# Kernel tuning notes

Hardware: AMD Instinct MI355X
Metric: run time of the kernel (lower is better)

## Reference

```python
import jax, jax.numpy as jnp
import numpy as np
from itertools import product as _prod

B = 2          # batch size
NPB = 4096     # voxels per batch
C = 384        # input_dim
H = 8          # num_heads
OUT = 32       # output_dim (seg classes)
SPATIAL = (32, 256, 256)
POOL_R = np.array([1, 2, 2, 2])    # [1]+query_gs_ratio
COMP_R = np.array([1, 16, 16, 16])  # [1]+compress_ratio


def _coords():
    rng = np.random.default_rng(0)
    rows = []
    for b in range(B):
        cand = np.stack([rng.integers(0, s, 4 * NPB) for s in SPATIAL], 1)
        cand = np.unique(cand, axis=0)
        sel = cand[rng.permutation(len(cand))[:NPB]]
        rows.append(np.concatenate([np.full((NPB, 1), b, np.int64), sel], 1))
    return np.concatenate(rows).astype(np.int32)


def setup_inputs() -> dict:
    idx = _coords()                     # [N,4] unique (b,z,y,x)
    N = idx.shape[0]
    pool_u, pool_inv = np.unique(idx // POOL_R, axis=0, return_inverse=True)
    emb_u, emb_inv = np.unique(idx // COMP_R, axis=0, return_inverse=True)
    # submanifold 3x3x3 neighbor table (same batch), -1 = missing
    lut = {tuple(r): i for i, r in enumerate(idx.tolist())}
    nbr = np.full((N, 27), -1, np.int32)
    rows = idx.tolist()
    for k, (dz, dy, dx) in enumerate(_prod((-1, 0, 1), repeat=3)):
        for i, (b, z, y, x) in enumerate(rows):
            nbr[i, k] = lut.get((b, z + dz, y + dy, x + dx), -1)
    key = jax.random.key(0)
    ks = jax.random.split(key, 12)
    g = lambda k, shp, s: jax.random.normal(k, shp, jnp.float32) * s
    s = 1.0 / float(np.sqrt(C))
    return dict(
        feats=g(ks[0], (N, C), 1.0),
        W_pool=g(ks[1], (C, C), s), b_pool=jnp.zeros((C,), jnp.float32),
        W_emb=g(ks[2], (C, C), s), b_emb=jnp.zeros((C,), jnp.float32),
        Wq=g(ks[3], (C, C), s), bq=jnp.zeros((C,), jnp.float32),
        Wk=g(ks[4], (C, C), s), bk=jnp.zeros((C,), jnp.float32),
        Wv=g(ks[5], (C, C), s), bv=jnp.zeros((C,), jnp.float32),
        Wo=g(ks[6], (C, C), s), bo=jnp.zeros((C,), jnp.float32),
        W_conv=g(ks[7], (27, C, OUT), 1.0 / float(np.sqrt(27 * C))),
        b_conv=jnp.zeros((OUT,), jnp.float32),
        pool_inv=jnp.asarray(pool_inv, jnp.int32),
        pool_coords=jnp.asarray(pool_u, jnp.int32),
        emb_inv=jnp.asarray(emb_inv, jnp.int32),
        emb_coords=jnp.asarray(emb_u, jnp.int32),
        nbr_idx=jnp.asarray(nbr),
        batch_size=B,
    )


def _sine_pe(xyz, d_pos):
    # xyz: [n,3] normalized to [0,1]; PositionEmbeddingCoordsSine (3detr-style)
    cdim = d_pos // xyz.shape[1]
    dim_t = 10000.0 ** (2.0 * (jnp.arange(cdim) // 2).astype(jnp.float32) / cdim)
    emb = (xyz * (2.0 * jnp.pi))[:, :, None] / dim_t          # [n,3,cdim]
    pe = jnp.stack([jnp.sin(emb[..., 0::2]), jnp.cos(emb[..., 1::2])], -1)
    return pe.reshape(xyz.shape[0], -1)                        # [n,d_pos]


def reference(feats, W_pool, b_pool, W_emb, b_emb, Wq, bq, Wk, bk, Wv, bv,
              Wo, bo, W_conv, b_conv, pool_inv, pool_coords, emb_inv,
              emb_coords, nbr_idx, batch_size):
    Mp, Me, Cc = pool_coords.shape[0], emb_coords.shape[0], feats.shape[1]
    hd = Cc // H
    # query path: linear + scatter_max over pool cells
    pool_f = jax.ops.segment_max(feats @ W_pool + b_pool, pool_inv, num_segments=Mp)
    # kv path: linear + scatter_max over compressed cells (coords of argmax rows
    # within a cell all equal the unique cell coord, so mean == unique coord)
    emb_f = jax.ops.segment_max(feats @ W_emb + b_emb, emb_inv, num_segments=Me)
    # per-batch min/max-normalized sine positional encoding on concat(emb,pool)
    emb_xyz = emb_coords[:, 1:].astype(jnp.float32)
    pool_xyz = pool_coords[:, 1:].astype(jnp.float32)
    all_xyz = jnp.concatenate([emb_xyz, pool_xyz], 0)
    bids = jnp.concatenate([emb_coords[:, 0], pool_coords[:, 0]], 0)
    mins = jax.ops.segment_min(all_xyz, bids, num_segments=batch_size)
    maxs = jax.ops.segment_max(all_xyz, bids, num_segments=batch_size)
    norm = (all_xyz - mins[bids]) / (maxs[bids] - mins[bids] + 1e-6)
    pe = _sine_pe(norm, Cc)
    emb_f = emb_f + pe[:Me]
    pool_f = pool_f + pe[Me:]
    # multi-head cross-attention, masked to same-batch pairs
    q = (pool_f @ Wq + bq).reshape(Mp, H, hd)
    k = (emb_f @ Wk + bk).reshape(Me, H, hd)
    v = (emb_f @ Wv + bv).reshape(Me, H, hd)
    scores = jnp.einsum('phd,ehd->hpe', q, k) / jnp.sqrt(jnp.float32(hd))
    same_b = pool_coords[:, 0][None, :, None] == emb_coords[:, 0][None, None, :]
    attn = jax.nn.softmax(jnp.where(same_b, scores, -1e9), axis=-1)
    o = jnp.einsum('hpe,ehd->phd', attn, v).reshape(Mp, Cc) @ Wo + bo
    # broadcast back to voxels + residual
    new_f = feats + o[pool_inv]
    # SubMConv3d seg head: gather 27 neighbors, contract with kernel
    valid = (nbr_idx >= 0)[:, :, None]
    gathered = jnp.where(valid, new_f[jnp.maximum(nbr_idx, 0)], 0.0)  # [N,27,C]
    logits = jnp.einsum('nkc,kco->no', gathered, W_conv) + b_conv
    return logits
```

## Files before the change

kernel.cpp:

```cpp
#include <hip/hip_runtime.h>
#include <hip/hip_bf16.h>
#include <math.h>

#define CDIM 384
#define NHEAD 8
#define HD 48
#define OUTD 32
#define MAXB 16
#define CONVK 10368

typedef __bf16 bf16x8 __attribute__((ext_vector_type(8)));
typedef float f32x4 __attribute__((ext_vector_type(4)));

__device__ __forceinline__ f32x4 mfma16(bf16x8 a, bf16x8 b, f32x4 c) {
  return __builtin_amdgcn_mfma_f32_16x16x32_bf16(a, b, c, 0, 0, 0);
}
__device__ __forceinline__ bf16x8 zero8() {
  bf16x8 z = {(__bf16)0.f, (__bf16)0.f, (__bf16)0.f, (__bf16)0.f,
              (__bf16)0.f, (__bf16)0.f, (__bf16)0.f, (__bf16)0.f};
  return z;
}

__device__ __forceinline__ unsigned enc_f(float f) {
  unsigned u = __float_as_uint(f);
  return (u & 0x80000000u) ? ~u : (u | 0x80000000u);
}
__device__ __forceinline__ float dec_f(unsigned u) {
  unsigned v = (u & 0x80000000u) ? (u ^ 0x80000000u) : ~u;
  return __uint_as_float(v);
}

__global__ void init_small_kernel(int* smin, int* smax, int* eb) {
  int t = threadIdx.x;
  if (t < MAXB * 3) { smin[t] = 0x7fffffff; smax[t] = (int)0x80000000; }
  if (t <= MAXB) eb[t] = 0;
}

__global__ __launch_bounds__(256) void prep_kernel(
    const float* __restrict__ feats, __hip_bfloat16* __restrict__ feats16, int N,
    const float* __restrict__ W_pool, const float* __restrict__ W_emb,
    const float* __restrict__ Wk, const float* __restrict__ Wv,
    const float* __restrict__ Wq, const float* __restrict__ Wo,
    __hip_bfloat16* __restrict__ Wt_pe, __hip_bfloat16* __restrict__ Wt_kv,
    __hip_bfloat16* __restrict__ Wt_q, __hip_bfloat16* __restrict__ Wt_o,
    const float* __restrict__ Wc, __hip_bfloat16* __restrict__ Wct,
    unsigned* __restrict__ encA, unsigned* __restrict__ encB,
    __hip_bfloat16* __restrict__ vt, int Mepad,
    const int* __restrict__ ec, const int* __restrict__ pc, int Mp, int Me,
    const int* __restrict__ bsz, int* smin, int* smax, int* ebv,
    int nbF, int nbW, int nbC, int nbZA, int nbZB, int nbVt, int nbM) {
  __shared__ int lmin[MAXB * 3], lmax[MAXB * 3];
  int b = blockIdx.x;
  int t = threadIdx.x;
  if (b < nbF) {
    int v = b * 256 + t;
    if (v < N * 48) {
      float4 a0 = *reinterpret_cast<const float4*>(feats + (size_t)v * 8);
      float4 a1 = *reinterpret_cast<const float4*>(feats + (size_t)v * 8 + 4);
      __hip_bfloat16 tmp[8] = {
        __float2bfloat16(a0.x), __float2bfloat16(a0.y), __float2bfloat16(a0.z), __float2bfloat16(a0.w),
        __float2bfloat16(a1.x), __float2bfloat16(a1.y), __float2bfloat16(a1.z), __float2bfloat16(a1.w)};
      *reinterpret_cast<bf16x8*>(feats16 + (size_t)v * 8) = *reinterpret_cast<const bf16x8*>(tmp);
    }
    return;
  }
  b -= nbF;
  if (b < 6 * nbW) {
    int m = b / nbW;
    int v = (b - m * nbW) * 256 + t;
    if (v >= CDIM * 48) return;
    const float* src;
    __hip_bfloat16* dst;
    switch (m) {
      case 0: src = W_pool; dst = Wt_pe; break;
      case 1: src = W_emb;  dst = Wt_pe + (size_t)CDIM * CDIM; break;
      case 2: src = Wk;     dst = Wt_kv; break;
      case 3: src = Wv;     dst = Wt_kv + (size_t)CDIM * CDIM; break;
      case 4: src = Wq;     dst = Wt_q; break;
      default: src = Wo;    dst = Wt_o; break;
    }
    int k8i = v / CDIM;
    int n = v - k8i * CDIM;
    int k8 = k8i * 8;
    __hip_bfloat16 tmp[8];
    #pragma unroll
    for (int u = 0; u < 8; ++u) tmp[u] = __float2bfloat16(src[(size_t)(k8 + u) * CDIM + n]);
    *reinterpret_cast<bf16x8*>(dst + (size_t)n * CDIM + k8) = *reinterpret_cast<const bf16x8*>(tmp);
    return;
  }
  b -= 6 * nbW;
  if (b < nbC) {
    int v = b * 256 + t;
    if (v >= OUTD * (CONVK / 8)) return;
    int k8i = v >> 5;
    int n = v & 31;
    int k8 = k8i * 8;
    __hip_bfloat16 tmp[8];
    #pragma unroll
    for (int u = 0; u < 8; ++u) tmp[u] = __float2bfloat16(Wc[(size_t)(k8 + u) * OUTD + n]);
    *reinterpret_cast<bf16x8*>(Wct + (size_t)n * CONVK + k8) = *reinterpret_cast<const bf16x8*>(tmp);
    return;
  }
  b -= nbC;
  if (b < nbZA) {
    size_t v = (size_t)b * 256 + t;
    if (v < (size_t)Mp * 96) {
      uint4 z = {0u, 0u, 0u, 0u};
      reinterpret_cast<uint4*>(encA)[v] = z;
    }
    return;
  }
  b -= nbZA;
  if (b < nbZB) {
    size_t v = (size_t)b * 256 + t;
    if (v < (size_t)Me * 96) {
      uint4 z = {0u, 0u, 0u, 0u};
      reinterpret_cast<uint4*>(encB)[v] = z;
    }
    return;
  }
  b -= nbZB;
  if (b < nbVt) {
    int v = b * 256 + t;
    int g = Mepad >> 3;
    if (v < 512 * g) {
      int row = v / g;
      int c8 = (v - row * g) * 8;
      __hip_bfloat16 bv = __float2bfloat16(((row & 63) == HD) ? 1.0f : 0.0f);
      __hip_bfloat16 tmp[8] = {bv, bv, bv, bv, bv, bv, bv, bv};
      *reinterpret_cast<bf16x8*>(vt + (size_t)row * Mepad + c8) =
          *reinterpret_cast<const bf16x8*>(tmp);
    }
    return;
  }
  b -= nbVt;
  if (b < nbM) {
    if (t < MAXB * 3) { lmin[t] = 0x7fffffff; lmax[t] = (int)0x80000000; }
    __syncthreads();
    int i = b * 256 + t;
    int tot = Me + Mp;
    if (i < tot) {
      const int* r = (i < Me) ? (ec + 4 * i) : (pc + 4 * (i - Me));
      int bb = r[0];
      #pragma unroll
      for (int d = 0; d < 3; ++d) {
        atomicMin(&lmin[bb * 3 + d], r[1 + d]);
        atomicMax(&lmax[bb * 3 + d], r[1 + d]);
      }
    }
    __syncthreads();
    if (t < MAXB * 3) {
      if (lmin[t] != 0x7fffffff) atomicMin(&smin[t], lmin[t]);
      if (lmax[t] != (int)0x80000000) atomicMax(&smax[t], lmax[t]);
    }
    return;
  }
  b -= nbM;
  {
    int e = b * 256 + t;
    if (e == 0) { ebv[0] = 0; ebv[bsz[0]] = Me; }
    if (e > 0 && e < Me) {
      int b0 = ec[4 * (e - 1)], b1 = ec[4 * e];
      for (int bb = b0 + 1; bb <= b1; ++bb) ebv[bb] = e;
    }
  }
}

__global__ void pe_kernel(const unsigned* __restrict__ encP, const unsigned* __restrict__ encE,
                          __hip_bfloat16* __restrict__ pool16, __hip_bfloat16* __restrict__ emb16,
                          const int* __restrict__ pc, int Mp,
                          const int* __restrict__ ec, int Me,
                          const int* __restrict__ smin, const int* __restrict__ smax) {
  int gid = blockIdx.x * blockDim.x + threadIdx.x;
  int total = (Mp + Me) * CDIM;
  if (gid >= total) return;
  int row = gid / CDIM, c = gid - row * CDIM;
  const int* coords;
  const unsigned* src;
  __hip_bfloat16* dst;
  int lrow;
  if (row < Me) { lrow = row; coords = ec + 4 * row; src = encE; dst = emb16; }
  else { lrow = row - Me; coords = pc + 4 * lrow; src = encP; dst = pool16; }
  int b = coords[0];
  int dim = c >> 7;
  int i = c & 127;
  int j = i >> 1;
  float x = (float)coords[1 + dim];
  float mn = (float)smin[b * 3 + dim];
  float mx = (float)smax[b * 3 + dim];
  float nrm = (x - mn) / (mx - mn + 1e-6f);
  float freq = exp2f(-(float)j * 0.20762050593046014f);
  float arg = nrm * 6.283185307179586f * freq;
  float pe = (i & 1) ? __cosf(arg) : __sinf(arg);
  float val = dec_f(src[(size_t)lrow * CDIM + c]) + pe;
  dst[(size_t)lrow * CDIM + c] = __float2bfloat16(val);
}

template <int EPI>
__device__ __forceinline__ void mgemm_body(
    int bx, int by,
    __hip_bfloat16 (*As)[72], __hip_bfloat16 (*Bs)[72],
    const __hip_bfloat16* __restrict__ A, int M,
    const __hip_bfloat16* __restrict__ Wt,
    const float* __restrict__ bias0, const float* __restrict__ bias1,
    void* __restrict__ d0, void* __restrict__ d1,
    const int* __restrict__ inv0, const int* __restrict__ inv1,
    int Mepad) {
  const int m0 = bx * 128;
  const int n0 = by * 64;
  const int t = threadIdx.x;
  const int lane = t & 63, w = t >> 6;
  const int wr = w >> 1, wc = w & 1;
  const int lq = lane & 15, lg = lane >> 4;

  f32x4 acc[4][2];
  #pragma unroll
  for (int i = 0; i < 4; ++i) {
    acc[i][0] = (f32x4){0.f, 0.f, 0.f, 0.f};
    acc[i][1] = (f32x4){0.f, 0.f, 0.f, 0.f};
  }
  const int arow = t >> 3;
  const int acol = (t & 7) * 8;

  for (int k0 = 0; k0 < CDIM; k0 += 64) {
    #pragma unroll
    for (int i = 0; i < 4; ++i) {
      int r = arow + i * 32;
      int gr = m0 + r;
      bf16x8 val = zero8();
      if (gr < M) val = *reinterpret_cast<const bf16x8*>(A + (size_t)gr * CDIM + k0 + acol);
      *reinterpret_cast<bf16x8*>(&As[r][acol]) = val;
    }
    #pragma unroll
    for (int i = 0; i < 2; ++i) {
      int r = arow + i * 32;
      bf16x8 val = *reinterpret_cast<const bf16x8*>(Wt + (size_t)(n0 + r) * CDIM + k0 + acol);
      *reinterpret_cast<bf16x8*>(&Bs[r][acol]) = val;
    }
    __syncthreads();
    #pragma unroll
    for (int ks = 0; ks < 2; ++ks) {
      bf16x8 af[4], bfv[2];
      #pragma unroll
      for (int fm = 0; fm < 4; ++fm)
        af[fm] = *reinterpret_cast<const bf16x8*>(&As[wr * 64 + fm * 16 + lq][ks * 32 + lg * 8]);
      #pragma unroll
      for (int fn = 0; fn < 2; ++fn)
        bfv[fn] = *reinterpret_cast<const bf16x8*>(&Bs[wc * 32 + fn * 16 + lq][ks * 32 + lg * 8]);
      #pragma unroll
      for (int fm = 0; fm < 4; ++fm)
        #pragma unroll
        for (int fn = 0; fn < 2; ++fn)
          acc[fm][fn] = mfma16(af[fm], bfv[fn], acc[fm][fn]);
    }
    __syncthreads();
  }

  const bool sec = (n0 >= CDIM);
  const int nb = n0 - (sec ? CDIM : 0) + wc * 32;
  const int nA = nb + lq, nB = nb + 16 + lq;

  if (EPI == 0) {
    const float* bias = sec ? bias1 : bias0;
    unsigned* dst = (unsigned*)(sec ? d1 : d0);
    const int* inv = sec ? inv1 : inv0;
    float bA = bias[nA], bB = bias[nB];
    #pragma unroll
    for (int fm = 0; fm < 4; ++fm) {
      int rbase = m0 + wr * 64 + fm * 16 + lg * 4;
      int cs = -1;
      float mA = 0.f, mB = 0.f;
      #pragma unroll
      for (int j = 0; j < 4; ++j) {
        int r = rbase + j;
        if (r < M) {
          int s = inv[r];
          float vA = acc[fm][0][j] + bA;
          float vB = acc[fm][1][j] + bB;
          if (s == cs) { mA = fmaxf(mA, vA); mB = fmaxf(mB, vB); }
          else {
            if (cs >= 0) {
              atomicMax(&dst[(size_t)cs * CDIM + nA], enc_f(mA));
              atomicMax(&dst[(size_t)cs * CDIM + nB], enc_f(mB));
            }
            cs = s; mA = vA; mB = vB;
          }
        }
      }
      if (cs >= 0) {
        atomicMax(&dst[(size_t)cs * CDIM + nA], enc_f(mA));
        atomicMax(&dst[(size_t)cs * CDIM + nB], enc_f(mB));
      }
    }
  } else if (EPI == 1) {
    float bA = bias0[nA], bB = bias0[nB];
    float* dst = (float*)d0;
    #pragma unroll
    for (int fm = 0; fm < 4; ++fm)
      #pragma unroll
      for (int j = 0; j < 4; ++j) {
        int r = m0 + wr * 64 + fm * 16 + lg * 4 + j;
        if (r < M) {
          dst[(size_t)r * CDIM + nA] = acc[fm][0][j] + bA;
          dst[(size_t)r * CDIM + nB] = acc[fm][1][j] + bB;
        }
      }
  } else if (EPI == 2) {
    const float scale = 0.2082350914f;
    float bA = bias0[nA], bB = bias0[nB];
    int hA = nA / HD, dA = nA - hA * HD;
    int hB = nB / HD, dB = nB - hB * HD;
    __hip_bfloat16* dst = (__hip_bfloat16*)d0;
    #pragma unroll
    for (int fm = 0; fm < 4; ++fm)
      #pragma unroll
      for (int j = 0; j < 4; ++j) {
        int r = m0 + wr * 64 + fm * 16 + lg * 4 + j;
        if (r < M) {
          dst[(size_t)r * 512 + hA * 64 + dA] = __float2bfloat16((acc[fm][0][j] + bA) * scale);
          dst[(size_t)r * 512 + hB * 64 + dB] = __float2bfloat16((acc[fm][1][j] + bB) * scale);
        }
      }
  } else {
    if (!sec) {
      float bA = bias0[nA], bB = bias0[nB];
      int hA = nA / HD, dA = nA - hA * HD;
      int hB = nB / HD, dB = nB - hB * HD;
      __hip_bfloat16* dst = (__hip_bfloat16*)d0;
      #pragma unroll
      for (int fm = 0; fm < 4; ++fm)
        #pragma unroll
        for (int j = 0; j < 4; ++j) {
          int r = m0 + wr * 64 + fm * 16 + lg * 4 + j;
          if (r < M) {
            dst[(size_t)r * 512 + hA * 64 + dA] = __float2bfloat16(acc[fm][0][j] + bA);
            dst[(size_t)r * 512 + hB * 64 + dB] = __float2bfloat16(acc[fm][1][j] + bB);
          }
        }
    } else {
      float bA = bias1[nA], bB = bias1[nB];
      int hA = nA / HD, dA = nA - hA * HD;
      int hB = nB / HD, dB = nB - hB * HD;
      __hip_bfloat16* dst = (__hip_bfloat16*)d1;
      #pragma unroll
      for (int fm = 0; fm < 4; ++fm)
        #pragma unroll
        for (int j = 0; j < 4; ++j) {
          int r = m0 + wr * 64 + fm * 16 + lg * 4 + j;
          if (r < M) {
            dst[(size_t)(hA * 64 + dA) * Mepad + r] = __float2bfloat16(acc[fm][0][j] + bA);
            dst[(size_t)(hB * 64 + dB) * Mepad + r] = __float2bfloat16(acc[fm][1][j] + bB);
          }
        }
    }
  }
  if ((EPI == 2 || EPI == 3) && n0 == 0) {
    __hip_bfloat16* dst = (__hip_bfloat16*)d0;
    for (int c = t; c < 1024; c += 256) {
      int r = m0 + (c >> 3);
      int hh = c & 7;
      if (r < M) {
        bf16x8 z = zero8();
        *reinterpret_cast<bf16x8*>(dst + (size_t)r * 512 + hh * 64 + 48) = z;
        *reinterpret_cast<bf16x8*>(dst + (size_t)r * 512 + hh * 64 + 56) = z;
      }
    }
  }
}

__global__ __launch_bounds__(256) void mgemm0_kernel(
    const __hip_bfloat16* __restrict__ A, int M, const __hip_bfloat16* __restrict__ Wt,
    const float* __restrict__ bias0, const float* __restrict__ bias1,
    unsigned* __restrict__ d0, unsigned* __restrict__ d1,
    const int* __restrict__ inv0, const int* __restrict__ inv1) {
  __shared__ __align__(16) __hip_bfloat16 As[128][72];
  __shared__ __align__(16) __hip_bfloat16 Bs[64][72];
  mgemm_body<0>(blockIdx.x, blockIdx.y, As, Bs, A, M, Wt, bias0, bias1, d0, d1, inv0, inv1, 0);
}

__global__ __launch_bounds__(256) void mgemm1_kernel(
    const __hip_bfloat16* __restrict__ A, int M, const __hip_bfloat16* __restrict__ Wt,
    const float* __restrict__ bias0, float* __restrict__ d0) {
  __shared__ __align__(16) __hip_bfloat16 As[128][72];
  __shared__ __align__(16) __hip_bfloat16 Bs[64][72];
  mgemm_body<1>(blockIdx.x, blockIdx.y, As, Bs, A, M, Wt, bias0, nullptr, d0, nullptr, nullptr, nullptr, 0);
}

__global__ __launch_bounds__(256) void qkv_kernel(
    const __hip_bfloat16* __restrict__ pool16, int Mp, const __hip_bfloat16* __restrict__ Wt_q,
    const float* __restrict__ bq,
    const __hip_bfloat16* __restrict__ emb16, int Me, const __hip_bfloat16* __restrict__ Wt_kv,
    const float* __restrict__ bk, const float* __restrict__ bv,
    __hip_bfloat16* __restrict__ q16, __hip_bfloat16* __restrict__ k16,
    __hip_bfloat16* __restrict__ vt, int Mepad, int nbQ, int gxQ, int gxK) {
  __shared__ __align__(16) __hip_bfloat16 As[128][72];
  __shared__ __align__(16) __hip_bfloat16 Bs[64][72];
  int b = blockIdx.x;
  if (b < nbQ) {
    mgemm_body<2>(b % gxQ, b / gxQ, As, Bs, pool16, Mp, Wt_q, bq, nullptr,
                  q16, nullptr, nullptr, nullptr, 0);
  } else {
    b -= nbQ;
    mgemm_body<3>(b % gxK, b / gxK, As, Bs, emb16, Me, Wt_kv, bk, bv,
                  k16, vt, nullptr, nullptr, Mepad);
  }
}

__global__ __launch_bounds__(256) void attn_mfma_kernel(
    const __hip_bfloat16* __restrict__ qb, const __hip_bfloat16* __restrict__ kb,
    const __hip_bfloat16* __restrict__ vt, int Mepad,
    const int* __restrict__ pc, const int* __restrict__ eb,
    int Mp, int Me, __hip_bfloat16* __restrict__ ob) {
  __shared__ __align__(16) __hip_bfloat16 Ks[2][64][72];
  __shared__ __align__(16) __hip_bfloat16 Vs[2][64][72];
  __shared__ __align__(16) __hip_bfloat16 pl[4][16][72];
  __shared__ int sred[4][4];
  const int h = blockIdx.y;
  const int t = threadIdx.x;
  const int wv = t >> 6, lane = t & 63;
  const int lq = lane & 15, lg = lane >> 4;
  const int q0 = blockIdx.x * 64 + wv * 16;

  int lo[4], hi[4];
  #pragma unroll
  for (int r = 0; r < 4; ++r) {
    int q = q0 + lg * 4 + r;
    if (q < Mp) { int b = pc[4 * q]; lo[r] = eb[b]; hi[r] = eb[b + 1]; }
    else { lo[r] = 0x7fffffff; hi[r] = 0; }
  }
  int lomin = min(min(lo[0], lo[1]), min(lo[2], lo[3]));
  int lomax = max(max(lo[0], lo[1]), max(lo[2], lo[3]));
  int himin = min(min(hi[0], hi[1]), min(hi[2], hi[3]));
  int himax = max(max(hi[0], hi[1]), max(hi[2], hi[3]));
  #pragma unroll
  for (int off = 1; off < 64; off <<= 1) {
    lomin = min(lomin, __shfl_xor(lomin, off));
    lomax = max(lomax, __shfl_xor(lomax, off));
    himin = min(himin, __shfl_xor(himin, off));
    himax = max(himax, __shfl_xor(himax, off));
  }
  if (lane == 0) {
    sred[wv][0] = lomin; sred[wv][1] = lomax;
    sred[wv][2] = himin; sred[wv][3] = himax;
  }
  __syncthreads();
  lomin = min(min(sred[0][0], sred[1][0]), min(sred[2][0], sred[3][0]));
  lomax = max(max(sred[0][1], sred[1][1]), max(sred[2][1], sred[3][1]));
  himin = min(min(sred[0][2], sred[1][2]), min(sred[2][2], sred[3][2]));
  himax = max(max(sred[0][3], sred[1][3]), max(sred[2][3], sred[3][3]));

  int qrow = min(q0 + lq, Mp - 1);
  const __hip_bfloat16* qp = qb + (size_t)qrow * 512 + h * 64 + lg * 8;
  bf16x8 aq0 = *reinterpret_cast<const bf16x8*>(qp);
  bf16x8 aq1 = *reinterpret_cast<const bf16x8*>(qp + 32);

  const int str = t >> 2;
  const int stc = (t & 3) * 16;
  const __hip_bfloat16* vrow = vt + (size_t)(h * 64 + str) * Mepad + stc;

  f32x4 zero = {0.f, 0.f, 0.f, 0.f};
  f32x4 oacc[4];
  oacc[0] = zero; oacc[1] = zero; oacc[2] = zero; oacc[3] = zero;

  bf16x8 k0, k1, v0, v1;
  auto load_tile = [&](int e0) {
    int er = e0 + str;
    k0 = zero8(); k1 = zero8();
    if (er < Me) {
      const __hip_bfloat16* kp = kb + (size_t)er * 512 + h * 64 + stc;
      k0 = *reinterpret_cast<const bf16x8*>(kp);
      k1 = *reinterpret_cast<const bf16x8*>(kp + 8);
    }
    v0 = *reinterpret_cast<const bf16x8*>(vrow + e0);
    v1 = *reinterpret_cast<const bf16x8*>(vrow + e0 + 8);
  };
  auto store_tile = [&](int nb) {
    *reinterpret_cast<bf16x8*>(&Ks[nb][str][stc]) = k0;
    *reinterpret_cast<bf16x8*>(&Ks[nb][str][stc + 8]) = k1;
    *reinterpret_cast<bf16x8*>(&Vs[nb][str][stc]) = v0;
    *reinterpret_cast<bf16x8*>(&Vs[nb][str][stc + 8]) = v1;
  };
  const int e0beg = lomin & ~63;
  load_tile(e0beg);
  store_tile(0);
  if (e0beg + 64 < himax) load_tile(e0beg + 64);

  int it = 0;
  for (int e0 = e0beg; e0 < himax; e0 += 64, ++it) {
    __syncthreads();
    const int cur = it & 1;
    if (e0 + 64 < himax) {
      store_tile(cur ^ 1);
      if (e0 + 128 < himax) load_tile(e0 + 128);
    }

    f32x4 sf[4];
    #pragma unroll
    for (int s = 0; s < 4; ++s) {
      bf16x8 bk0 = *reinterpret_cast<const bf16x8*>(&Ks[cur][s * 16 + lq][lg * 8]);
      bf16x8 bk1 = *reinterpret_cast<const bf16x8*>(&Ks[cur][s * 16 + lq][32 + lg * 8]);
      f32x4 z = zero;
      z = mfma16(aq0, bk0, z);
      z = mfma16(aq1, bk1, z);
      sf[s] = z;
    }
    const bool interior = (e0 >= lomax) && (e0 + 64 <= himin);
    if (interior) {
      #pragma unroll
      for (int s = 0; s < 4; ++s)
        #pragma unroll
        for (int r = 0; r < 4; ++r)
          pl[wv][lg * 4 + r][s * 16 + lq] = __float2bfloat16(exp2f(sf[s][r]));
    } else {
      #pragma unroll
      for (int s = 0; s < 4; ++s) {
        int e = e0 + s * 16 + lq;
        #pragma unroll
        for (int r = 0; r < 4; ++r) {
          bool m = (e >= lo[r]) && (e < hi[r]);
          float p = m ? exp2f(sf[s][r]) : 0.f;
          pl[wv][lg * 4 + r][s * 16 + lq] = __float2bfloat16(p);
        }
      }
    }
    asm volatile("s_waitcnt lgkmcnt(0)" ::: "memory");
    __builtin_amdgcn_sched_barrier(0);
    #pragma unroll
    for (int ks = 0; ks < 2; ++ks) {
      bf16x8 ap = *reinterpret_cast<const bf16x8*>(&pl[wv][lq][ks * 32 + lg * 8]);
      #pragma unroll
      for (int dt = 0; dt < 4; ++dt) {
        bf16x8 bv = *reinterpret_cast<const bf16x8*>(&Vs[cur][dt * 16 + lq][ks * 32 + lg * 8]);
        oacc[dt] = mfma16(ap, bv, oacc[dt]);
      }
    }
  }

  #pragma unroll
  for (int r = 0; r < 4; ++r) {
    float l = __shfl(oacc[3][r], (lane & 48));
    int q = q0 + lg * 4 + r;
    if (q < Mp && l > 0.f) {
      float inv = 1.0f / l;
      __hip_bfloat16* op = ob + (size_t)q * CDIM + h * HD;
      op[lq]      = __float2bfloat16(oacc[0][r] * inv);
      op[16 + lq] = __float2bfloat16(oacc[1][r] * inv);
      op[32 + lq] = __float2bfloat16(oacc[2][r] * inv);
    }
  }
}

__global__ void newf16_kernel(const float* __restrict__ feats, const float* __restrict__ o2,
                              const int* __restrict__ pinv, __hip_bfloat16* __restrict__ nf,
                              int N) {
  int v = blockIdx.x * 256 + threadIdx.x;
  if (v >= N * 48) return;
  int n = v / 48, c8 = (v - n * 48) * 8;
  const float* fp = feats + (size_t)n * CDIM + c8;
  const float* op = o2 + (size_t)pinv[n] * CDIM + c8;
  float4 a0 = *reinterpret_cast<const float4*>(fp);
  float4 a1 = *reinterpret_cast<const float4*>(fp + 4);
  float4 b0 = *reinterpret_cast<const float4*>(op);
  float4 b1 = *reinterpret_cast<const float4*>(op + 4);
  __hip_bfloat16 tmp[8] = {
    __float2bfloat16(a0.x + b0.x), __float2bfloat16(a0.y + b0.y),
    __float2bfloat16(a0.z + b0.z), __float2bfloat16(a0.w + b0.w),
    __float2bfloat16(a1.x + b1.x), __float2bfloat16(a1.y + b1.y),
    __float2bfloat16(a1.z + b1.z), __float2bfloat16(a1.w + b1.w)};
  *reinterpret_cast<bf16x8*>(nf + (size_t)v * 8) = *reinterpret_cast<const bf16x8*>(tmp);
}

__global__ __launch_bounds__(256) void mconv_kernel(
    const __hip_bfloat16* __restrict__ nf, const int* __restrict__ nbr,
    const __hip_bfloat16* __restrict__ Wct, float* __restrict__ outp, int N) {
  __shared__ __align__(16) __hip_bfloat16 As[128][72];
  __shared__ __align__(16) __hip_bfloat16 Bs[32][72];
  __shared__ int jrow[128];
  const int n0 = blockIdx.x * 128;
  const int kg = blockIdx.y;
  const int t = threadIdx.x;
  const int lane = t & 63, w = t >> 6;
  const int lq = lane & 15, lg = lane >> 4;
  f32x4 acc[2][2];
  acc[0][0] = (f32x4){0.f,0.f,0.f,0.f}; acc[0][1] = acc[0][0];
  acc[1][0] = acc[0][0]; acc[1][1] = acc[0][0];
  const int arow = t >> 3, acol = (t & 7) * 8;

  for (int kk = kg * 3; kk < kg * 3 + 3; ++kk) {
    __syncthreads();
    if (t < 128) {
      int n = n0 + t;
      jrow[t] = (n < N) ? nbr[(size_t)n * 27 + kk] : -1;
    }
    __syncthreads();
    for (int c0 = 0; c0 < CDIM; c0 += 64) {
      #pragma unroll
      for (int i = 0; i < 4; ++i) {
        int r = arow + i * 32;
        int j = jrow[r];
        bf16x8 val = zero8();
        if (j >= 0) val = *reinterpret_cast<const bf16x8*>(nf + (size_t)j * CDIM + c0 + acol);
        *reinterpret_cast<bf16x8*>(&As[r][acol]) = val;
      }
      {
        int r = t >> 3;
        bf16x8 val = *reinterpret_cast<const bf16x8*>(Wct + (size_t)r * CONVK + kk * CDIM + c0 + acol);
        *reinterpret_cast<bf16x8*>(&Bs[r][acol]) = val;
      }
      __syncthreads();
      #pragma unroll
      for (int ks = 0; ks < 2; ++ks) {
        bf16x8 af[2], bfv[2];
        #pragma unroll
        for (int fm = 0; fm < 2; ++fm)
          af[fm] = *reinterpret_cast<const bf16x8*>(&As[w * 32 + fm * 16 + lq][ks * 32 + lg * 8]);
        #pragma unroll
        for (int fn = 0; fn < 2; ++fn)
          bfv[fn] = *reinterpret_cast<const bf16x8*>(&Bs[fn * 16 + lq][ks * 32 + lg * 8]);
        #pragma unroll
        for (int fm = 0; fm < 2; ++fm)
          #pragma unroll
          for (int fn = 0; fn < 2; ++fn)
            acc[fm][fn] = mfma16(af[fm], bfv[fn], acc[fm][fn]);
      }
      __syncthreads();
    }
  }
  #pragma unroll
  for (int fm = 0; fm < 2; ++fm)
    #pragma unroll
    for (int j = 0; j < 4; ++j) {
      int r = n0 + w * 32 + fm * 16 + lg * 4 + j;
      if (r < N) {
        #pragma unroll
        for (int fn = 0; fn < 2; ++fn)
          outp[((size_t)kg * N + r) * OUTD + fn * 16 + lq] = acc[fm][fn][j];
      }
    }
}

__global__ void conv_reduce_kernel(const float* __restrict__ outp,
                                   const float* __restrict__ bc,
                                   float* __restrict__ out, int N) {
  int v = blockIdx.x * 256 + threadIdx.x;
  if (v >= N * OUTD) return;
  int oo = v & (OUTD - 1);
  float s = bc[oo];
  #pragma unroll
  for (int kg = 0; kg < 9; ++kg) s += outp[(size_t)kg * N * OUTD + v];
  out[v] = s;
}

extern "C" void kernel_launch(void* const* d_in, const int* in_sizes, int n_in,
                              void* d_out, int out_size, void* d_ws, size_t ws_size,
                              hipStream_t stream) {
  const float* feats  = (const float*)d_in[0];
  const float* W_pool = (const float*)d_in[1];
  const float* b_pool = (const float*)d_in[2];
  const float* W_emb  = (const float*)d_in[3];
  const float* b_emb  = (const float*)d_in[4];
  const float* Wq = (const float*)d_in[5];  const float* bq = (const float*)d_in[6];
  const float* Wk = (const float*)d_in[7];  const float* bk = (const float*)d_in[8];
  const float* Wv = (const float*)d_in[9];  const float* bv = (const float*)d_in[10];
  const float* Wo = (const float*)d_in[11]; const float* bo = (const float*)d_in[12];
  const float* Wc = (const float*)d_in[13]; const float* bc = (const float*)d_in[14];
  const int* pool_inv    = (const int*)d_in[15];
  const int* pool_coords = (const int*)d_in[16];
  const int* emb_inv     = (const int*)d_in[17];
  const int* emb_coords  = (const int*)d_in[18];
  const int* nbr         = (const int*)d_in[19];
  const int* bsz         = (const int*)d_in[20];
  int N  = in_sizes[0] / CDIM;
  int Mp = in_sizes[16] / 4;
  int Me = in_sizes[18] / 4;
  int Mepad = ((Me >> 6) + 2) << 6;

  char* wsb = (char*)d_ws;
  size_t off = 0;
  auto alloc = [&](size_t bytes) { void* p = wsb + off; off += (bytes + 255) & ~(size_t)255; return p; };
  unsigned* encA = (unsigned*)alloc((size_t)Mp * CDIM * 4);
  unsigned* encB = (unsigned*)alloc((size_t)Me * CDIM * 4);
  __hip_bfloat16* vt = (__hip_bfloat16*)alloc((size_t)512 * Mepad * 2);
  __hip_bfloat16* pool16  = (__hip_bfloat16*)alloc((size_t)Mp * CDIM * 2);
  __hip_bfloat16* emb16   = (__hip_bfloat16*)alloc((size_t)Me * CDIM * 2);
  __hip_bfloat16* feats16 = (__hip_bfloat16*)alloc((size_t)N * CDIM * 2);
  float* o2 = (float*)alloc((size_t)Mp * CDIM * 4 > (size_t)9 * N * OUTD * 4
                                ? (size_t)Mp * CDIM * 4 : (size_t)9 * N * OUTD * 4);
  __hip_bfloat16* Wt_pe = (__hip_bfloat16*)alloc((size_t)768 * CDIM * 2);
  __hip_bfloat16* Wt_kv = (__hip_bfloat16*)alloc((size_t)768 * CDIM * 2);
  __hip_bfloat16* Wt_q  = (__hip_bfloat16*)alloc((size_t)CDIM * CDIM * 2);
  __hip_bfloat16* Wt_o  = (__hip_bfloat16*)alloc((size_t)CDIM * CDIM * 2);
  __hip_bfloat16* Wct   = (__hip_bfloat16*)alloc((size_t)OUTD * CONVK * 2);
  int* smin = (int*)alloc(MAXB * 3 * 4);
  int* smax = (int*)alloc(MAXB * 3 * 4);
  int* eb   = (int*)alloc((MAXB + 1) * 4);

  __hip_bfloat16* q16  = (__hip_bfloat16*)encA;
  __hip_bfloat16* k16  = (__hip_bfloat16*)encB;
  __hip_bfloat16* ob16 = pool16;
  __hip_bfloat16* newf16 = feats16;
  float* outp = o2;

  init_small_kernel<<<1, 64, 0, stream>>>(smin, smax, eb);

  int nbF  = (N * 48 + 255) / 256;
  int nbW  = (CDIM * 48 + 255) / 256;
  int nbC  = (OUTD * (CONVK / 8) + 255) / 256;
  int nbZA = ((Mp * 96) + 255) / 256;
  int nbZB = ((Me * 96) + 255) / 256;
  int nbVt = ((512 * (Mepad >> 3)) + 255) / 256;
  int nbM  = (Mp + Me + 255) / 256;
  int nbE  = (Me + 255) / 256;
  prep_kernel<<<nbF + 6 * nbW + nbC + nbZA + nbZB + nbVt + nbM + nbE, 256, 0, stream>>>(
      feats, feats16, N, W_pool, W_emb, Wk, Wv, Wq, Wo,
      Wt_pe, Wt_kv, Wt_q, Wt_o, Wc, Wct, encA, encB, vt, Mepad,
      emb_coords, pool_coords, Mp, Me, bsz, smin, smax, eb,
      nbF, nbW, nbC, nbZA, nbZB, nbVt, nbM);

  mgemm0_kernel<<<dim3((N + 127) / 128, 12), 256, 0, stream>>>(
      feats16, N, Wt_pe, b_pool, b_emb, encA, encB, pool_inv, emb_inv);
  pe_kernel<<<((Mp + Me) * CDIM + 255) / 256, 256, 0, stream>>>(
      encA, encB, pool16, emb16, pool_coords, Mp, emb_coords, Me, smin, smax);

  {
    int gxQ = (Mp + 127) / 128, gxK = (Me + 127) / 128;
    int nbQ = gxQ * 6;
    qkv_kernel<<<nbQ + gxK * 12, 256, 0, stream>>>(
        pool16, Mp, Wt_q, bq, emb16, Me, Wt_kv, bk, bv,
        q16, k16, vt, Mepad, nbQ, gxQ, gxK);
  }

  attn_mfma_kernel<<<dim3((Mp + 63) / 64, NHEAD), 256, 0, stream>>>(
      q16, k16, vt, Mepad, pool_coords, eb, Mp, Me, ob16);

  mgemm1_kernel<<<dim3((Mp + 127) / 128, 6), 256, 0, stream>>>(
      ob16, Mp, Wt_o, bo, o2);

  newf16_kernel<<<(N * 48 + 255) / 256, 256, 0, stream>>>(feats, o2, pool_inv, newf16, N);

  mconv_kernel<<<dim3((N + 127) / 128, 9), 256, 0, stream>>>(newf16, nbr, Wct, outp, N);
  conv_reduce_kernel<<<(N * OUTD + 255) / 256, 256, 0, stream>>>(outp, bc, (float*)d_out, N);
}
```

Measured before the change: 158.9 us.

## Split attention key range across two blocks and merge partials in a combine kernel

Adds a grid z-dimension of two so each attention block handles half of the key tiles for its query group. Each half writes unnormalised fp32 partial outputs, including the denominator column, to a new workspace buffer. A new combine kernel adds the two partials and divides by the summed denominator to produce the bf16 output. The aim is to shorten each block's serial key loop and add parallelism, at the cost of an extra kernel launch and extra fp32 partial-output traffic.

```diff
diff --git a/kernel.cpp b/kernel.cpp
--- a/kernel.cpp
+++ b/kernel.cpp
@@ -358,11 +358,11 @@
     __hip_bfloat16* dst = (__hip_bfloat16*)d0;
     for (int c = t; c < 1024; c += 256) {
       int r = m0 + (c >> 3);
-      int hh = c & 7;
+      int hx = c & 7;
       if (r < M) {
         bf16x8 z = zero8();
-        *reinterpret_cast<bf16x8*>(dst + (size_t)r * 512 + hh * 64 + 48) = z;
-        *reinterpret_cast<bf16x8*>(dst + (size_t)r * 512 + hh * 64 + 56) = z;
+        *reinterpret_cast<bf16x8*>(dst + (size_t)r * 512 + hx * 64 + 48) = z;
+        *reinterpret_cast<bf16x8*>(dst + (size_t)r * 512 + hx * 64 + 56) = z;
       }
     }
   }
@@ -410,12 +410,13 @@
     const __hip_bfloat16* __restrict__ qb, const __hip_bfloat16* __restrict__ kb,
     const __hip_bfloat16* __restrict__ vt, int Mepad,
     const int* __restrict__ pc, const int* __restrict__ eb,
-    int Mp, int Me, __hip_bfloat16* __restrict__ ob) {
+    int Mp, int Me, float* __restrict__ po) {
   __shared__ __align__(16) __hip_bfloat16 Ks[2][64][72];
   __shared__ __align__(16) __hip_bfloat16 Vs[2][64][72];
   __shared__ __align__(16) __hip_bfloat16 pl[4][16][72];
   __shared__ int sred[4][4];
   const int h = blockIdx.y;
+  const int zz = blockIdx.z;
   const int t = threadIdx.x;
   const int wv = t >> 6, lane = t & 63;
   const int lq = lane & 15, lg = lane >> 4;
@@ -449,6 +450,12 @@
   himin = min(min(sred[0][2], sred[1][2]), min(sred[2][2], sred[3][2]));
   himax = max(max(sred[0][3], sred[1][3]), max(sred[2][3], sred[3][3]));
 
+  const int e0all = lomin & ~63;
+  const int nt = (himax > e0all) ? ((himax - e0all + 63) >> 6) : 0;
+  const int half = (nt + 1) >> 1;
+  const int s0 = e0all + zz * half * 64;
+  const int send = min(himax, e0all + (zz ? nt : half) * 64);
+
   int qrow = min(q0 + lq, Mp - 1);
   const __hip_bfloat16* qp = qb + (size_t)qrow * 512 + h * 64 + lg * 8;
   bf16x8 aq0 = *reinterpret_cast<const bf16x8*>(qp);
@@ -480,18 +487,19 @@
     *reinterpret_cast<bf16x8*>(&Vs[nb][str][stc]) = v0;
     *reinterpret_cast<bf16x8*>(&Vs[nb][str][stc + 8]) = v1;
   };
-  const int e0beg = lomin & ~63;
-  load_tile(e0beg);
-  store_tile(0);
-  if (e0beg + 64 < himax) load_tile(e0beg + 64);
+  if (s0 < send) {
+    load_tile(s0);
+    store_tile(0);
+    if (s0 + 64 < send) load_tile(s0 + 64);
+  }
 
   int it = 0;
-  for (int e0 = e0beg; e0 < himax; e0 += 64, ++it) {
+  for (int e0 = s0; e0 < send; e0 += 64, ++it) {
     __syncthreads();
     const int cur = it & 1;
-    if (e0 + 64 < himax) {
+    if (e0 + 64 < send) {
       store_tile(cur ^ 1);
-      if (e0 + 128 < himax) load_tile(e0 + 128);
+      if (e0 + 128 < send) load_tile(e0 + 128);
     }
 
     f32x4 sf[4];
@@ -538,16 +546,26 @@
 
   #pragma unroll
   for (int r = 0; r < 4; ++r) {
-    float l = __shfl(oacc[3][r], (lane & 48));
     int q = q0 + lg * 4 + r;
-    if (q < Mp && l > 0.f) {
-      float inv = 1.0f / l;
-      __hip_bfloat16* op = ob + (size_t)q * CDIM + h * HD;
-      op[lq]      = __float2bfloat16(oacc[0][r] * inv);
-      op[16 + lq] = __float2bfloat16(oacc[1][r] * inv);
-      op[32 + lq] = __float2bfloat16(oacc[2][r] * inv);
-    }
-  }
+    if (q < Mp) {
+      float* pp = po + (((size_t)zz * Mp + q) * NHEAD + h) * 64;
+      #pragma unroll
+      for (int dt = 0; dt < 4; ++dt) pp[dt * 16 + lq] = oacc[dt][r];
+    }
+  }
+}
+
+__global__ void combine_kernel(const float* __restrict__ po, int Mp,
+                               __hip_bfloat16* __restrict__ ob) {
+  int gid = blockIdx.x * 256 + threadIdx.x;
+  if (gid >= Mp * CDIM) return;
+  int q = gid / CDIM, c = gid - q * CDIM;
+  int h = c / HD, d = c - h * HD;
+  const float* p0 = po + (((size_t)q) * NHEAD + h) * 64;
+  const float* p1 = po + (((size_t)(Mp + q)) * NHEAD + h) * 64;
+  float l = p0[HD] + p1[HD];
+  float v = p0[d] + p1[d];
+  ob[(size_t)q * CDIM + c] = __float2bfloat16(l > 0.f ? v / l : 0.f);
 }
 
 __global__ void newf16_kernel(const float* __restrict__ feats, const float* __restrict__ o2,
@@ -691,6 +709,7 @@
   __hip_bfloat16* Wt_q  = (__hip_bfloat16*)alloc((size_t)CDIM * CDIM * 2);
   __hip_bfloat16* Wt_o  = (__hip_bfloat16*)alloc((size_t)CDIM * CDIM * 2);
   __hip_bfloat16* Wct   = (__hip_bfloat16*)alloc((size_t)OUTD * CONVK * 2);
+  float* po = (float*)alloc((size_t)2 * Mp * NHEAD * 64 * 4);
   int* smin = (int*)alloc(MAXB * 3 * 4);
   int* smax = (int*)alloc(MAXB * 3 * 4);
   int* eb   = (int*)alloc((MAXB + 1) * 4);
@@ -730,8 +749,9 @@
         q16, k16, vt, Mepad, nbQ, gxQ, gxK);
   }
 
-  attn_mfma_kernel<<<dim3((Mp + 63) / 64, NHEAD), 256, 0, stream>>>(
-      q16, k16, vt, Mepad, pool_coords, eb, Mp, Me, ob16);
+  attn_mfma_kernel<<<dim3((Mp + 63) / 64, NHEAD, 2), 256, 0, stream>>>(
+      q16, k16, vt, Mepad, pool_coords, eb, Mp, Me, po);
+  combine_kernel<<<(Mp * CDIM + 255) / 256, 256, 0, stream>>>(po, Mp, ob16);
 
   mgemm1_kernel<<<dim3((Mp + 127) / 128, 6), 256, 0, stream>>>(
       ob16, Mp, Wt_o, bo, o2);
```

New measurement: 168.4 us. 1.06x slower.
